# Performance work log

Hardware: AMD Instinct MI355X
Metric: run time of the kernel (lower is better)

The kernel has to match this reference:

```python
import jax, jax.numpy as jnp
import numpy as np
import math

B, S, E, H = 4, 2048, 1024, 16
D = E // H
INFINITY = 1000000.0

def setup_inputs() -> dict:
    key = jax.random.key(0)
    ks = jax.random.split(key, 10)
    std = 1.0 / math.sqrt(E)
    inp = {
        "x": jax.random.normal(ks[0], (B, S, E), dtype=jnp.float32),
        "mask": jax.random.randint(ks[1], (B, S), 0, 2).astype(jnp.bool_),
        "WQ_w": jax.random.uniform(ks[2], (E, E), jnp.float32, -std, std),
        "WQ_b": jax.random.uniform(ks[3], (E,), jnp.float32, -std, std),
        "WK_w": jax.random.uniform(ks[4], (E, E), jnp.float32, -std, std),
        "WK_b": jax.random.uniform(ks[5], (E,), jnp.float32, -std, std),
        "WV_w": jax.random.uniform(ks[6], (E, E), jnp.float32, -std, std),
        "WV_b": jax.random.uniform(ks[7], (E,), jnp.float32, -std, std),
        "WO_w": jax.random.uniform(ks[8], (E, E), jnp.float32, -std, std),
        "WO_b": jax.random.uniform(ks[9], (E,), jnp.float32, -std, std),
    }
    return inp

def reference(x, mask, WQ_w, WQ_b, WK_w, WK_b, WV_w, WV_b, WO_w, WO_b):
    # Linear layers: y = x @ W.T + b (torch convention)
    q = (x @ WQ_w.T + WQ_b).reshape(B, S, H, D).transpose(0, 2, 1, 3)  # (B,H,S,D)
    k = (x @ WK_w.T + WK_b).reshape(B, S, H, D).transpose(0, 2, 1, 3)
    v = (x @ WV_w.T + WV_b).reshape(B, S, H, D).transpose(0, 2, 1, 3)
    score = jnp.einsum("bhqd,bhkd->bhqk", q, k) / math.sqrt(D)  # (B,H,S,S)
    # additive key mask: -infinity where mask is False
    inv_mask = (~mask).astype(jnp.float32)[:, None, None, :]  # (B,1,1,S)
    score = score - inv_mask * INFINITY
    attn = jax.nn.softmax(score, axis=-1)
    o = jnp.einsum("bhqk,bhkd->bhqd", attn, v)  # (B,H,S,D)
    o = o.transpose(0, 2, 1, 3).reshape(B, S, E)
    o = o @ WO_w.T + WO_b
    o = jnp.abs(o * mask.astype(jnp.float32)[:, :, None])
    return o
```

## Files before the change

kernel.cpp:

```cpp
#include <hip/hip_runtime.h>
#include <math.h>

#define B_ 4
#define S_ 2048
#define E_ 1024
#define H_ 16
#define D_ 64
#define MTOT (B_*S_)

typedef _Float16 half8v __attribute__((ext_vector_type(8)));
typedef _Float16 half4v __attribute__((ext_vector_type(4)));
typedef float f32x4 __attribute__((ext_vector_type(4)));
typedef float f32x16 __attribute__((ext_vector_type(16)));
typedef unsigned uint4v __attribute__((ext_vector_type(4)));

typedef __attribute__((address_space(1))) const void gconst_void;
typedef __attribute__((address_space(3))) void lds_void;

#define MFMA16(a,b,c) __builtin_amdgcn_mfma_f32_16x16x32_f16((a),(b),(c),0,0,0)
#define MFMA32(a,b,c) __builtin_amdgcn_mfma_f32_32x32x16_f16((a),(b),(c),0,0,0)

#define QSCALE 0.18033688011112042f

static __device__ __forceinline__ unsigned cvt_pk_u32(float a, float b) {
  return __builtin_bit_cast(unsigned, __builtin_amdgcn_cvt_pkrtz(a, b));
}

#if __has_builtin(__builtin_amdgcn_permlane32_swap)
static __device__ __forceinline__ void pl32_swap(unsigned a, unsigned b,
                                                 unsigned& rlo, unsigned& rhi) {
  auto r = __builtin_amdgcn_permlane32_swap(a, b, false, false);
  rlo = r[0]; rhi = r[1];
}
#else
static __device__ __forceinline__ void pl32_swap(unsigned a, unsigned b,
                                                 unsigned& rlo, unsigned& rhi) {
  const int hi = (threadIdx.x & 63) >> 5;
  unsigned t = __shfl_xor(hi ? a : b, 32);
  rlo = hi ? t : a;
  rhi = hi ? b : t;
}
#endif

static __device__ __forceinline__ float partner32(float v, int hi) {
  unsigned u = __builtin_bit_cast(unsigned, v);
  unsigned lo_, hi_;
  pl32_swap(u, u, lo_, hi_);
  return __builtin_bit_cast(float, hi ? lo_ : hi_);
}

__global__ __launch_bounds__(256) void cvt_w4(const float* __restrict__ w0, const float* __restrict__ w1,
                                              const float* __restrict__ w2, const float* __restrict__ w3,
                                              _Float16* __restrict__ o0, _Float16* __restrict__ o1,
                                              _Float16* __restrict__ o2, _Float16* __restrict__ o3) {
  const int z = blockIdx.y;
  const float* in = (z == 0) ? w0 : (z == 1) ? w1 : (z == 2) ? w2 : w3;
  _Float16* out = (z == 0) ? o0 : (z == 1) ? o1 : (z == 2) ? o2 : o3;
  int i = (blockIdx.x * 256 + threadIdx.x) * 4;
  float4 v = *(const float4*)(in + i);
  half4v o;
  o[0] = (_Float16)v.x; o[1] = (_Float16)v.y; o[2] = (_Float16)v.z; o[3] = (_Float16)v.w;
  *(half4v*)(out + i) = o;
}

__global__ __launch_bounds__(256) void mask_prep(const unsigned char* __restrict__ mraw,
                                                 _Float16* __restrict__ maskc,
                                                 float* __restrict__ qmask,
                                                 int* __restrict__ ks,
                                                 int* __restrict__ nkpa) {
  __shared__ int flags[2];
  __shared__ int psum[256];
  const int b = blockIdx.x, tid = threadIdx.x;
  if (tid < 2) flags[tid] = 1;
  __syncthreads();
  const unsigned int* w = (const unsigned int*)mraw;
  for (int i = tid; i < 2048; i += 256) {
    unsigned int v = w[i];
    if (!(v == 0u || v == 1u)) flags[0] = 0;
    if (!(v == 0u || v == 0x3f800000u)) flags[1] = 0;
  }
  __syncthreads();
  const int is_i32 = flags[0], is_f32 = flags[1];
  int m[8]; int cnt = 0;
  for (int i = 0; i < 8; ++i) {
    const int idx = b * 2048 + tid * 8 + i;
    int mv;
    if (is_i32)      mv = ((const int*)mraw)[idx];
    else if (is_f32) mv = (((const unsigned int*)mraw)[idx] != 0u);
    else             mv = (mraw[idx] != 0);
    m[i] = mv; cnt += mv;
    qmask[idx] = mv ? 1.0f : 0.0f;
  }
  psum[tid] = cnt;
  __syncthreads();
  for (int off = 1; off < 256; off <<= 1) {
    int u = (tid >= off) ? psum[tid - off] : 0;
    __syncthreads();
    psum[tid] += u;
    __syncthreads();
  }
  const int total = psum[255];
  int base = psum[tid] - cnt;
  for (int i = 0; i < 8; ++i)
    if (m[i]) ks[b * 2048 + (base++)] = tid * 8 + i;
  for (int j = tid; j < 2048; j += 256)
    maskc[b * 2048 + j] = (j < total) ? (_Float16)0.0f : (_Float16)(-60000.0f);
  __syncthreads();
  const int lastv = (total > 0) ? ks[b * 2048 + total - 1] : 0;
  for (int j = total + tid; j < 2048; j += 256)
    ks[b * 2048 + j] = lastv;
  if (tid == 0) nkpa[b] = (total + 127) & ~127;
}

__global__ __launch_bounds__(256) void cvt_xc(const float* __restrict__ x,
                                              const int* __restrict__ ks,
                                              const int* __restrict__ nkpa,
                                              _Float16* __restrict__ xc) {
  const int b = blockIdx.y, j = blockIdx.x;
  if (j >= nkpa[b]) return;
  const int s = ks[b * 2048 + j];
  const float* src = x + (size_t)(b * 2048 + s) * E_;
  _Float16* dst = xc + (size_t)(b * 2048 + j) * E_;
  const int i = threadIdx.x * 4;
  float4 v = *(const float4*)(src + i);
  half4v o;
  o[0] = (_Float16)v.x; o[1] = (_Float16)v.y; o[2] = (_Float16)v.z; o[3] = (_Float16)v.w;
  *(half4v*)(dst + i) = o;
}

__device__ __forceinline__ void stage128x32(const _Float16* __restrict__ g, int ld,
                                            _Float16* lds, int wid, int lane) {
#pragma unroll
  for (int j = 0; j < 2; ++j) {
    const int c = j * 256 + wid * 64 + lane;
    const _Float16* src = g + (size_t)(c >> 2) * ld + (c & 3) * 8;
    _Float16* dst = lds + (size_t)(j * 256 + wid * 64) * 8;
    __builtin_amdgcn_global_load_lds((gconst_void*)src, (lds_void*)dst, 16, 0, 0);
  }
}

__global__ __launch_bounds__(256) void qkv_gemm(
    const _Float16* __restrict__ xc, const int* __restrict__ nkpa,
    const _Float16* __restrict__ wq, const _Float16* __restrict__ wk, const _Float16* __restrict__ wv,
    const float* __restrict__ bq, const float* __restrict__ bkp, const float* __restrict__ bvp,
    _Float16* __restrict__ Qc, _Float16* __restrict__ Kc, _Float16* __restrict__ Vc) {
  const int bx = blockIdx.x;
  const int bb = bx >> 4, tt = bx & 15;
  if (tt * 128 >= nkpa[bb]) return;
  __shared__ _Float16 As[128 * 32];
  __shared__ _Float16 Bs[128 * 32];
  const int tid = threadIdx.x, lane = tid & 63, wid = tid >> 6;
  const int g = lane >> 4, r16 = lane & 15;
  const int bm = bx * 128, bn = blockIdx.y * 128;
  const int z = blockIdx.z;
  const _Float16* w = (z == 0) ? wq : (z == 1) ? wk : wv;
  const float* bias = (z == 0) ? bq : (z == 1) ? bkp : bvp;
  const int wr = wid >> 1, wc = wid & 1;
  f32x4 acc[4][4] = {};
  for (int k0 = 0; k0 < E_; k0 += 32) {
    stage128x32(xc + (size_t)bm * E_ + k0, E_, As, wid, lane);
    stage128x32(w + (size_t)bn * E_ + k0, E_, Bs, wid, lane);
    __syncthreads();
    half8v a[4], bf[4];
#pragma unroll
    for (int i = 0; i < 4; ++i) a[i] = *(const half8v*)&As[(wr * 64 + i * 16 + r16) * 32 + g * 8];
#pragma unroll
    for (int i = 0; i < 4; ++i) bf[i] = *(const half8v*)&Bs[(wc * 64 + i * 16 + r16) * 32 + g * 8];
#pragma unroll
    for (int i = 0; i < 4; ++i)
#pragma unroll
      for (int j = 0; j < 4; ++j) acc[i][j] = MFMA16(a[i], bf[j], acc[i][j]);
    __syncthreads();
  }
#pragma unroll
  for (int i = 0; i < 4; ++i) {
#pragma unroll
    for (int j = 0; j < 4; ++j) {
      const int gn = bn + wc * 64 + j * 16 + r16;
      const float bb2 = bias[gn];
      const int h = gn >> 6, d = gn & 63;
      const int gm0 = bm + wr * 64 + i * 16 + g * 4;
      const int b_ = gm0 >> 11, s0 = gm0 & (S_ - 1);
      const size_t bhbase = (size_t)(b_ * H_ + h) * S_ * D_;
      if (z == 2) {
        half4v v4;
#pragma unroll
        for (int ii = 0; ii < 4; ++ii) v4[ii] = (_Float16)(acc[i][j][ii] + bb2);
        *(half4v*)&Vc[bhbase + (size_t)(s0 >> 4) * (D_ * 16) + d * 16 + (s0 & 15)] = v4;
      } else if (z == 1) {
#pragma unroll
        for (int ii = 0; ii < 4; ++ii) {
          const int s = s0 + ii;
          Kc[bhbase + (size_t)(s >> 5) * 2048 + (d >> 4) * 512 + (s & 31) * 16 + (d & 15)] =
              (_Float16)(acc[i][j][ii] + bb2);
        }
      } else {
#pragma unroll
        for (int ii = 0; ii < 4; ++ii)
          Qc[bhbase + (size_t)(s0 + ii) * D_ + d] = (_Float16)((acc[i][j][ii] + bb2) * QSCALE);
      }
    }
  }
}

__global__ __launch_bounds__(512) void attn_kernel(
    const _Float16* __restrict__ Qc, const _Float16* __restrict__ Kc, const _Float16* __restrict__ Vc,
    const _Float16* __restrict__ maskc, const int* __restrict__ ks, const int* __restrict__ nkpa,
    _Float16* __restrict__ Oh) {
  __shared__ float mlds[4][64][36];
  _Float16* smask = (_Float16*)&mlds[0][0][0];
  const int tid = threadIdx.x, lane = tid & 63, wid = tid >> 6;
  const int c = lane & 31, hi = lane >> 5;
  const int qg = wid & 3, kh = wid >> 2;
  const int id = blockIdx.x;
  const int slot = id & 7, rest = id >> 3;
  const int t = rest & 15, hbh = rest >> 4;
  const int hb = hbh * 8 + slot;
  const int b = hb >> 4, h = hb & 15;
  const int nkp = nkpa[b];
  if (t * 128 >= nkp) return;
  const size_t bh = (size_t)(b * H_ + h);
  const _Float16* Qb = Qc + bh * S_ * D_;
  const _Float16* Kb = Kc + bh * S_ * D_;
  const _Float16* Vb = Vc + bh * S_ * D_;

  *((half4v*)smask + tid) = *((const half4v*)(maskc + (size_t)b * S_) + tid);

  const int jq = t * 128 + qg * 32 + c;
  const int qs = ks[b * 2048 + jq];

  half8v qb[4];
#pragma unroll
  for (int kc = 0; kc < 4; ++kc)
    qb[kc] = *(const half8v*)&Qb[(size_t)jq * D_ + 16 * kc + 8 * hi];

  half8v bone = {};
  if (hi == 0) bone[0] = (_Float16)1.0f;
  const f32x16 fzero = {};

  f32x16 oacc[2] = {};
  float mrun = -1e30f, lrun = 0.f;
  const int laneoff = c * 16 + 8 * hi;
  const int nkh = nkp >> 1;
  const int kb0 = kh * nkh;

  __syncthreads();

  half8v kaf[4];
  {
    const _Float16* ktb = Kb + (size_t)(kb0 >> 5) * 2048 + laneoff;
#pragma unroll
    for (int kc = 0; kc < 4; ++kc) kaf[kc] = *(const half8v*)&ktb[kc * 512];
  }
  _Float16 mv = smask[kb0 + c];

  for (int kb = kb0; kb < kb0 + nkh; kb += 32) {
    half8v amask = {};
    if (hi == 0) amask[0] = mv;
    __builtin_amdgcn_s_setprio(1);
    f32x16 sc = MFMA32(amask, bone, fzero);
    sc = MFMA32(kaf[0], qb[0], sc);
    sc = MFMA32(kaf[1], qb[1], sc);
    sc = MFMA32(kaf[2], qb[2], sc);
    sc = MFMA32(kaf[3], qb[3], sc);
    __builtin_amdgcn_s_setprio(0);
    const int kbn = (kb + 32 < kb0 + nkh) ? kb + 32 : kb0;
    {
      const _Float16* ktb = Kb + (size_t)(kbn >> 5) * 2048 + laneoff;
#pragma unroll
      for (int kc = 0; kc < 4; ++kc) kaf[kc] = *(const half8v*)&ktb[kc * 512];
    }
    mv = smask[kbn + c];
    const _Float16* v_base = Vb + (size_t)(kb >> 4) * (D_ * 16) + laneoff;
    half8v va00 = *(const half8v*)&v_base[0];
    half8v va01 = *(const half8v*)&v_base[512];
    half8v va10 = *(const half8v*)&v_base[1024];
    half8v va11 = *(const half8v*)&v_base[1024 + 512];
    float t0 = fmaxf(sc[0], sc[4]), t1 = fmaxf(sc[1], sc[5]);
    float t2 = fmaxf(sc[2], sc[6]), t3 = fmaxf(sc[3], sc[7]);
    t0 = fmaxf(fmaxf(sc[8], sc[12]), t0);
    t1 = fmaxf(fmaxf(sc[9], sc[13]), t1);
    t2 = fmaxf(fmaxf(sc[10], sc[14]), t2);
    t3 = fmaxf(fmaxf(sc[11], sc[15]), t3);
    float pmax = fmaxf(fmaxf(t0, t1), fmaxf(t2, t3));
    pmax = fmaxf(pmax, partner32(pmax, hi));
    if (__any(pmax > mrun + 11.0f)) {
      float mnew = fmaxf(mrun, pmax);
      float corr = __builtin_amdgcn_exp2f(mrun - mnew);
      mrun = mnew;
      lrun *= corr;
#pragma unroll
      for (int dt = 0; dt < 2; ++dt)
#pragma unroll
        for (int r = 0; r < 16; ++r) oacc[dt][r] *= corr;
    }
    float ps0 = 0.f, ps1 = 0.f;
#pragma unroll
    for (int sl = 0; sl < 2; ++sl) {
      const int bs = 8 * sl;
      float p0 = __builtin_amdgcn_exp2f(sc[bs + 0] - mrun);
      float p1 = __builtin_amdgcn_exp2f(sc[bs + 1] - mrun);
      float p2 = __builtin_amdgcn_exp2f(sc[bs + 2] - mrun);
      float p3 = __builtin_amdgcn_exp2f(sc[bs + 3] - mrun);
      float p4 = __builtin_amdgcn_exp2f(sc[bs + 4] - mrun);
      float p5 = __builtin_amdgcn_exp2f(sc[bs + 5] - mrun);
      float p6 = __builtin_amdgcn_exp2f(sc[bs + 6] - mrun);
      float p7 = __builtin_amdgcn_exp2f(sc[bs + 7] - mrun);
      ps0 += (p0 + p1) + (p2 + p3);
      ps1 += (p4 + p5) + (p6 + p7);
      unsigned uA = cvt_pk_u32(p0, p1);
      unsigned uB = cvt_pk_u32(p2, p3);
      unsigned uC = cvt_pk_u32(p4, p5);
      unsigned uD = cvt_pk_u32(p6, p7);
      unsigned w0, w1, w2, w3;
      pl32_swap(uA, uC, w0, w2);
      pl32_swap(uB, uD, w1, w3);
      uint4v u4 = {w0, w1, w2, w3};
      half8v pb = __builtin_bit_cast(half8v, u4);
      __builtin_amdgcn_s_setprio(1);
      oacc[0] = MFMA32(sl ? va10 : va00, pb, oacc[0]);
      oacc[1] = MFMA32(sl ? va11 : va01, pb, oacc[1]);
      __builtin_amdgcn_s_setprio(0);
    }
    lrun += ps0 + ps1;
  }
  lrun += partner32(lrun, hi);
  __syncthreads();
  if (kh == 1) {
    float* p = &mlds[qg][lane][0];
#pragma unroll
    for (int dt = 0; dt < 2; ++dt)
#pragma unroll
      for (int rr = 0; rr < 4; ++rr) {
        float4 v4 = make_float4(oacc[dt][4 * rr], oacc[dt][4 * rr + 1],
                                oacc[dt][4 * rr + 2], oacc[dt][4 * rr + 3]);
        *(float4*)&p[dt * 16 + rr * 4] = v4;
      }
    p[32] = mrun;
    p[33] = lrun;
  }
  __syncthreads();
  if (kh == 0) {
    const float* p = &mlds[qg][lane][0];
    const float mB = p[32], lB = p[33];
    const float mS = fmaxf(mrun, mB);
    const float cA = __builtin_amdgcn_exp2f(mrun - mS);
    const float cB = __builtin_amdgcn_exp2f(mB - mS);
    const float inv = 1.0f / (lrun * cA + lB * cB);
    const float fA = cA * inv, fB = cB * inv;
    _Float16* orow = Oh + ((size_t)(b * S_ + qs)) * E_ + h * D_;
#pragma unroll
    for (int dt = 0; dt < 2; ++dt)
#pragma unroll
      for (int rr = 0; rr < 4; ++rr) {
        float4 vB = *(const float4*)&p[dt * 16 + rr * 4];
        half4v o4;
        o4[0] = (_Float16)(oacc[dt][4 * rr + 0] * fA + vB.x * fB);
        o4[1] = (_Float16)(oacc[dt][4 * rr + 1] * fA + vB.y * fB);
        o4[2] = (_Float16)(oacc[dt][4 * rr + 2] * fA + vB.z * fB);
        o4[3] = (_Float16)(oacc[dt][4 * rr + 3] * fA + vB.w * fB);
        *(half4v*)&orow[32 * dt + 8 * rr + 4 * hi] = o4;
      }
  }
}

__global__ __launch_bounds__(256) void oproj_gemm(
    const _Float16* __restrict__ Oh, const _Float16* __restrict__ wo, const float* __restrict__ bo,
    const float* __restrict__ qmask, float* __restrict__ out) {
  __shared__ _Float16 As[128 * 32];
  __shared__ _Float16 Bs[128 * 32];
  const int tid = threadIdx.x, lane = tid & 63, wid = tid >> 6;
  const int g = lane >> 4, r16 = lane & 15;
  const int bm = blockIdx.x * 128, bn = blockIdx.y * 128;
  const int wr = wid >> 1, wc = wid & 1;
  f32x4 acc[4][4] = {};
  for (int k0 = 0; k0 < E_; k0 += 32) {
    stage128x32(Oh + (size_t)bm * E_ + k0, E_, As, wid, lane);
    stage128x32(wo + (size_t)bn * E_ + k0, E_, Bs, wid, lane);
    __syncthreads();
    half8v a[4], bf[4];
#pragma unroll
    for (int i = 0; i < 4; ++i) a[i] = *(const half8v*)&As[(wr * 64 + i * 16 + r16) * 32 + g * 8];
#pragma unroll
    for (int i = 0; i < 4; ++i) bf[i] = *(const half8v*)&Bs[(wc * 64 + i * 16 + r16) * 32 + g * 8];
#pragma unroll
    for (int i = 0; i < 4; ++i)
#pragma unroll
      for (int j = 0; j < 4; ++j) acc[i][j] = MFMA16(a[i], bf[j], acc[i][j]);
    __syncthreads();
  }
#pragma unroll
  for (int i = 0; i < 4; ++i) {
#pragma unroll
    for (int j = 0; j < 4; ++j) {
      const int gn = bn + wc * 64 + j * 16 + r16;
      const float bb = bo[gn];
      const int gm0 = bm + wr * 64 + i * 16 + g * 4;
#pragma unroll
      for (int ii = 0; ii < 4; ++ii) {
        const int gm = gm0 + ii;
        const float y = acc[i][j][ii] + bb;
        out[(size_t)gm * E_ + gn] = fabsf(y * qmask[gm]);
      }
    }
  }
}

extern "C" void kernel_launch(void* const* d_in, const int* in_sizes, int n_in,
                              void* d_out, int out_size, void* d_ws, size_t ws_size,
                              hipStream_t stream) {
  const float* x = (const float*)d_in[0];
  const unsigned char* mask = (const unsigned char*)d_in[1];
  const float* WQ_w = (const float*)d_in[2];
  const float* WQ_b = (const float*)d_in[3];
  const float* WK_w = (const float*)d_in[4];
  const float* WK_b = (const float*)d_in[5];
  const float* WV_w = (const float*)d_in[6];
  const float* WV_b = (const float*)d_in[7];
  const float* WO_w = (const float*)d_in[8];
  const float* WO_b = (const float*)d_in[9];

  char* ws = (char*)d_ws;
  size_t off = 0;
  _Float16* xc  = (_Float16*)(ws + off); off += (size_t)MTOT * E_ * 2;
  _Float16* wqh = (_Float16*)(ws + off); off += (size_t)E_ * E_ * 2;
  _Float16* wkh = (_Float16*)(ws + off); off += (size_t)E_ * E_ * 2;
  _Float16* wvh = (_Float16*)(ws + off); off += (size_t)E_ * E_ * 2;
  _Float16* woh = (_Float16*)(ws + off); off += (size_t)E_ * E_ * 2;
  _Float16* Qc  = (_Float16*)(ws + off); off += (size_t)MTOT * E_ * 2;
  _Float16* Kc  = (_Float16*)(ws + off); off += (size_t)MTOT * E_ * 2;
  _Float16* Vc  = (_Float16*)(ws + off); off += (size_t)MTOT * E_ * 2;
  _Float16* Obuf = (_Float16*)(ws + off); off += (size_t)MTOT * E_ * 2;
  _Float16* maskcf = (_Float16*)(ws + off); off += (size_t)B_ * S_ * 2;
  float* qmaskf = (float*)(ws + off); off += (size_t)B_ * S_ * 4;
  int* ksl      = (int*)(ws + off); off += (size_t)B_ * S_ * 4;
  int* nkpa     = (int*)(ws + off); off += 64;
  if (ws_size < off) return;

  const int NW = E_ * E_;
  mask_prep<<<dim3(B_), dim3(256), 0, stream>>>(mask, maskcf, qmaskf, ksl, nkpa);
  cvt_w4<<<dim3(NW / 4 / 256, 4), dim3(256), 0, stream>>>(WQ_w, WK_w, WV_w, WO_w,
                                                          wqh, wkh, wvh, woh);
  cvt_xc<<<dim3(S_, B_), dim3(256), 0, stream>>>(x, ksl, nkpa, xc);
  qkv_gemm<<<dim3(MTOT / 128, E_ / 128, 3), dim3(256), 0, stream>>>(
      xc, nkpa, wqh, wkh, wvh, WQ_b, WK_b, WV_b, Qc, Kc, Vc);
  attn_kernel<<<dim3((S_ / 128) * H_ * B_), dim3(512), 0, stream>>>(
      Qc, Kc, Vc, maskcf, ksl, nkpa, Obuf);
  oproj_gemm<<<dim3(MTOT / 128, E_ / 128), dim3(256), 0, stream>>>(Obuf, woh, WO_b, qmaskf, (float*)d_out);
}
```

Before: 152.2 us.

## Compact masked-out query rows through oproj and scatter outputs to original positions

The attention output now stays in compacted row order. The output projection skips row tiles beyond the number of valid positions and scatters each result row back to its original sequence position through the ks permutation. A new zero_out kernel clears the whole output so masked rows read as zero. The qkv and attention grids are reordered so the tile index is the slowest-varying part of the block id, which lets skipped tiles cluster at the end of the launch. This trades about half the oproj GEMM work for an extra full-output memset and scattered row writes.

```diff
diff --git a/kernel.cpp b/kernel.cpp
--- a/kernel.cpp
+++ b/kernel.cpp
@@ -61,6 +61,12 @@
   half4v o;
   o[0] = (_Float16)v.x; o[1] = (_Float16)v.y; o[2] = (_Float16)v.z; o[3] = (_Float16)v.w;
   *(half4v*)(out + i) = o;
+}
+
+__global__ __launch_bounds__(256) void zero_out(float* __restrict__ out) {
+  const size_t i = ((size_t)blockIdx.x * 256 + threadIdx.x) * 4;
+  float4 z = make_float4(0.f, 0.f, 0.f, 0.f);
+  *(float4*)(out + i) = z;
 }
 
 __global__ __launch_bounds__(256) void mask_prep(const unsigned char* __restrict__ mraw,
@@ -144,15 +150,18 @@
     const _Float16* __restrict__ wq, const _Float16* __restrict__ wk, const _Float16* __restrict__ wv,
     const float* __restrict__ bq, const float* __restrict__ bkp, const float* __restrict__ bvp,
     _Float16* __restrict__ Qc, _Float16* __restrict__ Kc, _Float16* __restrict__ Vc) {
-  const int bx = blockIdx.x;
-  const int bb = bx >> 4, tt = bx & 15;
+  const int id = blockIdx.x;
+  const int tt = id / 96;
+  const int rem = id % 96;
+  const int bb = rem / 24;
+  const int r2 = rem % 24;
+  const int by = r2 / 3, z = r2 % 3;
   if (tt * 128 >= nkpa[bb]) return;
   __shared__ _Float16 As[128 * 32];
   __shared__ _Float16 Bs[128 * 32];
   const int tid = threadIdx.x, lane = tid & 63, wid = tid >> 6;
   const int g = lane >> 4, r16 = lane & 15;
-  const int bm = bx * 128, bn = blockIdx.y * 128;
-  const int z = blockIdx.z;
+  const int bm = (bb * 16 + tt) * 128, bn = by * 128;
   const _Float16* w = (z == 0) ? wq : (z == 1) ? wk : wv;
   const float* bias = (z == 0) ? bq : (z == 1) ? bkp : bvp;
   const int wr = wid >> 1, wc = wid & 1;
@@ -205,16 +214,15 @@
 
 __global__ __launch_bounds__(512) void attn_kernel(
     const _Float16* __restrict__ Qc, const _Float16* __restrict__ Kc, const _Float16* __restrict__ Vc,
-    const _Float16* __restrict__ maskc, const int* __restrict__ ks, const int* __restrict__ nkpa,
-    _Float16* __restrict__ Oh) {
+    const _Float16* __restrict__ maskc, const int* __restrict__ nkpa,
+    _Float16* __restrict__ Oc) {
   __shared__ float mlds[4][64][36];
   _Float16* smask = (_Float16*)&mlds[0][0][0];
   const int tid = threadIdx.x, lane = tid & 63, wid = tid >> 6;
   const int c = lane & 31, hi = lane >> 5;
   const int qg = wid & 3, kh = wid >> 2;
   const int id = blockIdx.x;
-  const int slot = id & 7, rest = id >> 3;
-  const int t = rest & 15, hbh = rest >> 4;
+  const int slot = id & 7, hbh = (id >> 3) & 7, t = id >> 6;
   const int hb = hbh * 8 + slot;
   const int b = hb >> 4, h = hb & 15;
   const int nkp = nkpa[b];
@@ -227,7 +235,6 @@
   *((half4v*)smask + tid) = *((const half4v*)(maskc + (size_t)b * S_) + tid);
 
   const int jq = t * 128 + qg * 32 + c;
-  const int qs = ks[b * 2048 + jq];
 
   half8v qb[4];
 #pragma unroll
@@ -348,7 +355,7 @@
     const float cB = __builtin_amdgcn_exp2f(mB - mS);
     const float inv = 1.0f / (lrun * cA + lB * cB);
     const float fA = cA * inv, fB = cB * inv;
-    _Float16* orow = Oh + ((size_t)(b * S_ + qs)) * E_ + h * D_;
+    _Float16* orow = Oc + ((size_t)(b * S_ + jq)) * E_ + h * D_;
 #pragma unroll
     for (int dt = 0; dt < 2; ++dt)
 #pragma unroll
@@ -365,17 +372,22 @@
 }
 
 __global__ __launch_bounds__(256) void oproj_gemm(
-    const _Float16* __restrict__ Oh, const _Float16* __restrict__ wo, const float* __restrict__ bo,
-    const float* __restrict__ qmask, float* __restrict__ out) {
+    const _Float16* __restrict__ Oc, const _Float16* __restrict__ wo, const float* __restrict__ bo,
+    const int* __restrict__ ks, const int* __restrict__ nkpa, float* __restrict__ out) {
+  const int id = blockIdx.x;
+  const int tt = id / 32;
+  const int rem = id % 32;
+  const int bb = rem / 8, by = rem % 8;
+  if (tt * 128 >= nkpa[bb]) return;
   __shared__ _Float16 As[128 * 32];
   __shared__ _Float16 Bs[128 * 32];
   const int tid = threadIdx.x, lane = tid & 63, wid = tid >> 6;
   const int g = lane >> 4, r16 = lane & 15;
-  const int bm = blockIdx.x * 128, bn = blockIdx.y * 128;
+  const int bm = (bb * 16 + tt) * 128, bn = by * 128;
   const int wr = wid >> 1, wc = wid & 1;
   f32x4 acc[4][4] = {};
   for (int k0 = 0; k0 < E_; k0 += 32) {
-    stage128x32(Oh + (size_t)bm * E_ + k0, E_, As, wid, lane);
+    stage128x32(Oc + (size_t)bm * E_ + k0, E_, As, wid, lane);
     stage128x32(wo + (size_t)bn * E_ + k0, E_, Bs, wid, lane);
     __syncthreads();
     half8v a[4], bf[4];
@@ -394,13 +406,15 @@
 #pragma unroll
     for (int j = 0; j < 4; ++j) {
       const int gn = bn + wc * 64 + j * 16 + r16;
-      const float bb = bo[gn];
+      const float bb2 = bo[gn];
       const int gm0 = bm + wr * 64 + i * 16 + g * 4;
 #pragma unroll
       for (int ii = 0; ii < 4; ++ii) {
         const int gm = gm0 + ii;
-        const float y = acc[i][j][ii] + bb;
-        out[(size_t)gm * E_ + gn] = fabsf(y * qmask[gm]);
+        const int b_ = gm >> 11, j_ = gm & (S_ - 1);
+        const int sorig = ks[b_ * 2048 + j_];
+        const float y = acc[i][j][ii] + bb2;
+        out[((size_t)(b_ * S_ + sorig)) * E_ + gn] = fabsf(y);
       }
     }
   }
@@ -430,7 +444,7 @@
   _Float16* Qc  = (_Float16*)(ws + off); off += (size_t)MTOT * E_ * 2;
   _Float16* Kc  = (_Float16*)(ws + off); off += (size_t)MTOT * E_ * 2;
   _Float16* Vc  = (_Float16*)(ws + off); off += (size_t)MTOT * E_ * 2;
-  _Float16* Obuf = (_Float16*)(ws + off); off += (size_t)MTOT * E_ * 2;
+  _Float16* Oc  = (_Float16*)(ws + off); off += (size_t)MTOT * E_ * 2;
   _Float16* maskcf = (_Float16*)(ws + off); off += (size_t)B_ * S_ * 2;
   float* qmaskf = (float*)(ws + off); off += (size_t)B_ * S_ * 4;
   int* ksl      = (int*)(ws + off); off += (size_t)B_ * S_ * 4;
@@ -442,9 +456,10 @@
   cvt_w4<<<dim3(NW / 4 / 256, 4), dim3(256), 0, stream>>>(WQ_w, WK_w, WV_w, WO_w,
                                                           wqh, wkh, wvh, woh);
   cvt_xc<<<dim3(S_, B_), dim3(256), 0, stream>>>(x, ksl, nkpa, xc);
-  qkv_gemm<<<dim3(MTOT / 128, E_ / 128, 3), dim3(256), 0, stream>>>(
+  zero_out<<<dim3(MTOT * E_ / 4 / 256), dim3(256), 0, stream>>>((float*)d_out);
+  qkv_gemm<<<dim3(16 * B_ * 8 * 3), dim3(256), 0, stream>>>(
       xc, nkpa, wqh, wkh, wvh, WQ_b, WK_b, WV_b, Qc, Kc, Vc);
   attn_kernel<<<dim3((S_ / 128) * H_ * B_), dim3(512), 0, stream>>>(
-      Qc, Kc, Vc, maskcf, ksl, nkpa, Obuf);
-  oproj_gemm<<<dim3(MTOT / 128, E_ / 128), dim3(256), 0, stream>>>(Obuf, woh, WO_b, qmaskf, (float*)d_out);
-}
+      Qc, Kc, Vc, maskcf, nkpa, Oc);
+  oproj_gemm<<<dim3(16 * B_ * 8), dim3(256), 0, stream>>>(Oc, woh, WO_b, ksl, nkpa, (float*)d_out);
+}
```

Measured after the change: 150.6 us. No clear change (-1.1%).
